# Kernel optimization log

Hardware: AMD Instinct MI355X
Metric: run time of the kernel (lower is better)

The kernel has to match this reference:

```python
import jax, jax.numpy as jnp
import numpy as np

EMBED = 1024
HEADS = 16
HEAD_DIM = EMBED // HEADS
MAX_REL = 16


def setup_inputs() -> dict:
    key = jax.random.key(0)
    ks = jax.random.split(key, 8)
    s = 0.02
    x = jax.random.normal(ks[0], (4, 2048, EMBED), dtype=jnp.float32)
    Wq = jax.random.normal(ks[1], (EMBED, EMBED), dtype=jnp.float32) * s
    bq = jnp.zeros((EMBED,), dtype=jnp.float32)
    Wk = jax.random.normal(ks[2], (EMBED, EMBED), dtype=jnp.float32) * s
    bk = jnp.zeros((EMBED,), dtype=jnp.float32)
    Wv = jax.random.normal(ks[3], (EMBED, EMBED), dtype=jnp.float32) * s
    bv = jnp.zeros((EMBED,), dtype=jnp.float32)
    rel_bias = jax.random.normal(ks[4], (2 * MAX_REL + 1, HEADS), dtype=jnp.float32) * s
    return {"x": x, "Wq": Wq, "bq": bq, "Wk": Wk, "bk": bk, "Wv": Wv, "bv": bv, "rel_bias": rel_bias}


def reference(x, Wq, bq, Wk, bk, Wv, bv, rel_bias):
    B, S, _ = x.shape
    # projections (Linear: x @ W + b, with W stored [in, out])
    q = (x @ Wq + bq).reshape(B, S, HEADS, HEAD_DIM).transpose(0, 2, 1, 3)  # [B,H,S,D]
    k = (x @ Wk + bk).reshape(B, S, HEADS, HEAD_DIM).transpose(0, 2, 1, 3)
    v = (x @ Wv + bv).reshape(B, S, HEADS, HEAD_DIM).transpose(0, 2, 1, 3)
    scores = jnp.einsum('bhqd,bhkd->bhqk', q, k) / jnp.sqrt(jnp.float32(HEAD_DIM))
    pos = jnp.arange(S)
    rel = jnp.clip(pos[None, :] - pos[:, None], -MAX_REL, MAX_REL) + MAX_REL  # [S,S]
    bias = rel_bias[rel]                      # [S,S,H]
    scores = scores + bias.transpose(2, 0, 1)[None]  # [B,H,S,S]
    probs = jax.nn.softmax(scores, axis=-1)
    # dropout is identity in eval mode
    out = jnp.einsum('bhqk,bhkd->bhqd', probs, v)
    return out.transpose(0, 2, 1, 3).reshape(B, S, EMBED)
```

## Files before the change

### kernel.cpp

```cpp
#include <hip/hip_runtime.h>

#define EMBED 1024
#define HEADS 16
#define HDIM  64
#define SEQ   2048
#define BATCH 4
#define MTOT  (BATCH*SEQ)

typedef __attribute__((ext_vector_type(8)))  short short8;
typedef __attribute__((ext_vector_type(4)))  float f32x4;
typedef __attribute__((ext_vector_type(16))) float f32x16;

#define GLOAD_LDS16(g, l) \
  __builtin_amdgcn_global_load_lds((const __attribute__((address_space(1))) void*)(g), \
                                   (__attribute__((address_space(3))) void*)(l), 16, 0, 0)

__device__ inline unsigned short f2bf(float f) {
  union { float f; unsigned u; } v; v.f = f;
  unsigned r = v.u + 0x7FFF + ((v.u >> 16) & 1);
  return (unsigned short)(r >> 16);
}

__device__ inline unsigned cvtpk(float lo, float hi) {
  unsigned r;
  asm("v_cvt_pk_bf16_f32 %0, %1, %2" : "=v"(r) : "v"(lo), "v"(hi));
  return r;
}

__device__ inline float vexp2(float x) {
  float r;
  asm("v_exp_f32 %0, %1" : "=v"(r) : "v"(x));
  return r;
}

#define PLSWAP(a, b) asm("v_permlane32_swap_b32 %0, %1" : "+v"(a), "+v"(b))

__device__ inline short8 mk8(unsigned w0, unsigned w1, unsigned w2, unsigned w3) {
  union { unsigned u[4]; short8 s; } x;
  x.u[0] = w0; x.u[1] = w1; x.u[2] = w2; x.u[3] = w3;
  return x.s;
}

__global__ void cvt_x(const float* __restrict__ x, unsigned short* __restrict__ xb) {
  int i = (blockIdx.x * blockDim.x + threadIdx.x) * 8;
  f32x4 a = *(const f32x4*)(x + i);
  f32x4 b = *(const f32x4*)(x + i + 4);
  unsigned short o[8];
  o[0]=f2bf(a[0]); o[1]=f2bf(a[1]); o[2]=f2bf(a[2]); o[3]=f2bf(a[3]);
  o[4]=f2bf(b[0]); o[5]=f2bf(b[1]); o[6]=f2bf(b[2]); o[7]=f2bf(b[3]);
  *(short8*)(xb + i) = *(short8*)o;
}

__global__ void transpose_w(const float* __restrict__ Wq, const float* __restrict__ Wk,
                            const float* __restrict__ Wv, unsigned short* __restrict__ Wtb) {
  __shared__ float tile[32][33];
  int wsel = blockIdx.z;
  const float* W = wsel == 0 ? Wq : (wsel == 1 ? Wk : Wv);
  int k0 = blockIdx.x * 32, n0 = blockIdx.y * 32;
  int tx = threadIdx.x & 31, ty = threadIdx.x >> 5;
  for (int i = 0; i < 4; ++i)
    tile[ty + i*8][tx] = W[(k0 + ty + i*8) * EMBED + n0 + tx];
  __syncthreads();
  unsigned short* o = Wtb + wsel * EMBED * EMBED;
  for (int i = 0; i < 4; ++i)
    o[(n0 + ty + i*8) * EMBED + k0 + tx] = f2bf(tile[tx][ty + i*8]);
}

__global__ __launch_bounds__(256)
void qkv_gemm(const unsigned short* __restrict__ xb, const unsigned short* __restrict__ Wtb,
              const float* __restrict__ bq, const float* __restrict__ bk, const float* __restrict__ bv,
              unsigned short* __restrict__ Qb, unsigned short* __restrict__ Kb,
              unsigned short* __restrict__ Vt) {
  __shared__ unsigned short As[128 * 72];
  __shared__ unsigned short Bs[128 * 72];
  int wsel = blockIdx.z;
  int m0 = blockIdx.x * 128, n0 = blockIdx.y * 128;
  int t = threadIdx.x, lane = t & 63, wave = t >> 6;
  int wr = wave >> 1, wc = wave & 1;
  int lr = lane & 15, lg = lane >> 4;
  const unsigned short* Wt = Wtb + wsel * (EMBED * EMBED);
  const float* bias = wsel == 0 ? bq : (wsel == 1 ? bk : bv);

  f32x4 acc[4][4] = {};

  for (int kt = 0; kt < EMBED / 64; ++kt) {
    int k0 = kt * 64;
    for (int i = 0; i < 4; ++i) {
      int c = i * 256 + t;
      int row = c >> 3, col8 = c & 7;
      short8 va = *(const short8*)(xb + (m0 + row) * EMBED + k0 + col8 * 8);
      short8 vb = *(const short8*)(Wt + (n0 + row) * EMBED + k0 + col8 * 8);
      *(short8*)(As + row * 72 + col8 * 8) = va;
      *(short8*)(Bs + row * 72 + col8 * 8) = vb;
    }
    __syncthreads();
    for (int kk = 0; kk < 2; ++kk) {
      short8 af[4], bfr[4];
      for (int mf = 0; mf < 4; ++mf)
        af[mf] = *(const short8*)(As + (wr * 64 + mf * 16 + lr) * 72 + kk * 32 + lg * 8);
      for (int nf = 0; nf < 4; ++nf)
        bfr[nf] = *(const short8*)(Bs + (wc * 64 + nf * 16 + lr) * 72 + kk * 32 + lg * 8);
      for (int mf = 0; mf < 4; ++mf)
        for (int nf = 0; nf < 4; ++nf)
          acc[mf][nf] = __builtin_amdgcn_mfma_f32_16x16x32_bf16(af[mf], bfr[nf], acc[mf][nf], 0, 0, 0);
    }
    __syncthreads();
  }

  const float SCLQ = 0.125f * 1.44269504088896340736f;
  for (int nf = 0; nf < 4; ++nf) {
    int n = n0 + wc * 64 + nf * 16 + lr;
    float bval = bias[n];
    int h = n >> 6, d = n & 63;
    for (int mf = 0; mf < 4; ++mf) {
      for (int r = 0; r < 4; ++r) {
        int m = m0 + wr * 64 + mf * 16 + lg * 4 + r;
        int b = m >> 11, s = m & 2047;
        float oval = acc[mf][nf][r] + bval;
        if (wsel == 0) oval *= SCLQ;
        unsigned short bfv = f2bf(oval);
        if (wsel == 0)      Qb[((b * HEADS + h) * SEQ + s) * HDIM + d] = bfv;
        else if (wsel == 1) Kb[((b * HEADS + h) * SEQ + s) * HDIM + d] = bfv;
        else                Vt[((b * HEADS + h) * HDIM + d) * SEQ + s] = bfv;
      }
    }
  }
}

__global__ __launch_bounds__(256)
void attn(const unsigned short* __restrict__ Qb, const unsigned short* __restrict__ Kb,
          const unsigned short* __restrict__ Vt, const float* __restrict__ rel_bias,
          float* __restrict__ out) {
  __shared__ unsigned short KVs[24576];
  __shared__ float bias_l[33];
  __shared__ float dld[4][32];
  int lid = ((blockIdx.x & 7) << 7) + (blockIdx.x >> 3);
  int bh = lid >> 4;
  int qb = lid & 15;
  int b = bh >> 4, h = bh & 15;
  int t = threadIdx.x, lane = t & 63, wave = t >> 6;
  int l31 = lane & 31, hi = lane >> 5;
  const float LOG2E = 1.44269504088896340736f;
  if (t < 33) bias_l[t] = rel_bias[t * HEADS + h] * LOG2E;

  int qw0 = qb * 128 + wave * 32;
  const unsigned short* Qp = Qb + (bh * SEQ + qw0) * HDIM;
  const unsigned short* Kp = Kb + bh * SEQ * HDIM;
  const unsigned short* Vp = Vt + bh * HDIM * SEQ;

  short8 qf[4];
  #pragma unroll
  for (int ks = 0; ks < 4; ++ks)
    qf[ks] = *(const short8*)(Qp + l31 * HDIM + ks * 16 + hi * 8);

  unsigned rbo[2][4];
  #pragma unroll
  for (int rs = 0; rs < 2; ++rs)
    #pragma unroll
    for (int ks = 0; ks < 4; ++ks) {
      int row = rs * 32 + l31;
      rbo[rs][ks] = (unsigned)((row << 7) + ((((ks << 1) | hi) ^ (row & 7)) << 4));
    }
  #define LDK(rs, ks, BUF) \
    (*(const short8*)((const char*)KVs + rbo[rs][ks] + (BUF) * 8192))
  #define LDVv(rs, ks, BUF) \
    (*(const short8*)((const char*)KVs + rbo[rs][ks] + 24576 + (BUF) * 8192))

  f32x16 O0 = {}, O1 = {};
  float ls0 = 0.f, ls1 = 0.f;
  int q = qw0 + l31;

  int srow0 = (wave << 4) + (lane >> 3);
  int sslot = lane & 7;

  #define STAGE(BUF, key0_)                                                          \
    for (int j = 0; j < 2; ++j) {                                                    \
      int srow = srow0 + j * 8;                                                      \
      int cs = sslot ^ (srow & 7);                                                   \
      GLOAD_LDS16(Kp + ((key0_) + srow) * HDIM + cs * 8,                             \
                  (char*)KVs + (BUF) * 8192 + ((((wave << 4) + j * 8) << 6) << 1));  \
      GLOAD_LDS16(Vp + srow * SEQ + (key0_) + cs * 8,                                \
                  (char*)KVs + 24576 + (BUF) * 8192 + ((((wave << 4) + j * 8) << 6) << 1)); \
    }

  #define WAITV4 asm volatile("s_waitcnt vmcnt(4)" ::: "memory");
  #define WAITV0 asm volatile("s_waitcnt vmcnt(0)" ::: "memory");
  #define BAR    __builtin_amdgcn_s_barrier();

  float cbLo, cbHi;

  #define PROC(SACC, KOFF, BUF)  {                                                   \
    float pv[16];                                                                    \
    int kbase = key0 + (KOFF);                                                       \
    if (kbase >= qw0 + 47) {                                                         \
      _Pragma("unroll") for (int r = 0; r < 16; ++r)                                 \
        pv[r] = vexp2(SACC[r] + cbHi);                                               \
    } else if (kbase <= qw0 - 47) {                                                  \
      _Pragma("unroll") for (int r = 0; r < 16; ++r)                                 \
        pv[r] = vexp2(SACC[r] + cbLo);                                               \
    } else {                                                                         \
      _Pragma("unroll") for (int r = 0; r < 16; ++r) {                               \
        int key = kbase + (r & 3) + 8 * (r >> 2) + 4 * hi;                           \
        int rel = key - q;                                                           \
        rel = rel < -16 ? -16 : (rel > 16 ? 16 : rel);                               \
        pv[r] = vexp2(SACC[r] + bias_l[rel + 16]);                                   \
      }                                                                              \
    }                                                                                \
    ls0 += ((pv[0] + pv[1]) + (pv[2] + pv[3])) + ((pv[4] + pv[5]) + (pv[6] + pv[7]));\
    ls1 += ((pv[8] + pv[9]) + (pv[10] + pv[11])) + ((pv[12] + pv[13]) + (pv[14] + pv[15]));\
    unsigned a0 = cvtpk(pv[0], pv[1]),  a1 = cvtpk(pv[4], pv[5]);   PLSWAP(a0, a1);  \
    unsigned a2 = cvtpk(pv[2], pv[3]),  a3 = cvtpk(pv[6], pv[7]);   PLSWAP(a2, a3);  \
    unsigned b0 = cvtpk(pv[8], pv[9]),  b1 = cvtpk(pv[12], pv[13]); PLSWAP(b0, b1);  \
    unsigned b2 = cvtpk(pv[10], pv[11]), b3 = cvtpk(pv[14], pv[15]); PLSWAP(b2, b3); \
    short8 pa0 = mk8(a0, a2, a1, a3);                                                \
    short8 pa1 = mk8(b0, b2, b1, b3);                                                \
    __builtin_amdgcn_s_setprio(1);                                                   \
    O0 = __builtin_amdgcn_mfma_f32_32x32x16_bf16(pa0, LDVv(0, (KOFF)/16, BUF),     O0, 0, 0, 0); \
    O1 = __builtin_amdgcn_mfma_f32_32x32x16_bf16(pa0, LDVv(1, (KOFF)/16, BUF),     O1, 0, 0, 0); \
    O0 = __builtin_amdgcn_mfma_f32_32x32x16_bf16(pa1, LDVv(0, (KOFF)/16 + 1, BUF), O0, 0, 0, 0); \
    O1 = __builtin_amdgcn_mfma_f32_32x32x16_bf16(pa1, LDVv(1, (KOFF)/16 + 1, BUF), O1, 0, 0, 0); \
    __builtin_amdgcn_s_setprio(0);                                                   \
  }

  #define HALF(RS, KOFF, BUF)  {                                                     \
    f32x16 s_ = {};                                                                  \
    __builtin_amdgcn_s_setprio(1);                                                   \
    _Pragma("unroll") for (int ks = 0; ks < 4; ++ks)                                 \
      s_ = __builtin_amdgcn_mfma_f32_32x32x16_bf16(LDK(RS, ks, BUF), qf[ks], s_, 0, 0, 0); \
    __builtin_amdgcn_s_setprio(0);                                                   \
    PROC(s_, KOFF, BUF)                                                              \
  }

  #define COMPUTE(BUF, KEY0)  {                                                      \
    int key0 = (KEY0);                                                               \
    HALF(0, 0, BUF)                                                                  \
    HALF(1, 32, BUF)                                                                 \
  }

  STAGE(0, 0)
  STAGE(1, 64)
  WAITV4
  __syncthreads();
  cbLo = bias_l[0]; cbHi = bias_l[32];

  for (int i = 0; i < 10; ++i) {
    int t3 = i * 3;
    STAGE(2, (t3 + 2) * 64)  COMPUTE(0, t3 * 64)        WAITV4 BAR
    STAGE(0, (t3 + 3) * 64)  COMPUTE(1, (t3 + 1) * 64)  WAITV4 BAR
    STAGE(1, (t3 + 4) * 64)  COMPUTE(2, (t3 + 2) * 64)  WAITV4 BAR
  }
  COMPUTE(0, 30 * 64)
  WAITV0 BAR
  COMPUTE(1, 31 * 64)

  float lsum = ls0 + ls1;
  float denom = lsum + __shfl_xor(lsum, 32, 64);
  if (lane < 32) dld[wave][l31] = 1.0f / denom;
  float* op = out + (b * SEQ + qw0) * EMBED + h * HDIM;
  #pragma unroll
  for (int r = 0; r < 16; ++r) {
    int ql = (r & 3) + 8 * (r >> 2) + 4 * hi;
    float inv = dld[wave][ql];
    op[ql * EMBED + l31]      = O0[r] * inv;
    op[ql * EMBED + 32 + l31] = O1[r] * inv;
  }
  #undef STAGE
  #undef LDK
  #undef LDVv
  #undef PROC
  #undef HALF
  #undef COMPUTE
}

extern "C" void kernel_launch(void* const* d_in, const int* in_sizes, int n_in,
                              void* d_out, int out_size, void* d_ws, size_t ws_size,
                              hipStream_t stream) {
  const float* x        = (const float*)d_in[0];
  const float* Wq       = (const float*)d_in[1];
  const float* bq       = (const float*)d_in[2];
  const float* Wk       = (const float*)d_in[3];
  const float* bk       = (const float*)d_in[4];
  const float* Wv       = (const float*)d_in[5];
  const float* bv       = (const float*)d_in[6];
  const float* rel_bias = (const float*)d_in[7];
  float* out = (float*)d_out;

  char* ws = (char*)d_ws;
  unsigned short* xb  = (unsigned short*)(ws);
  unsigned short* Wtb = (unsigned short*)(ws + 16777216);
  unsigned short* Qb  = (unsigned short*)(ws + 23068672);
  unsigned short* Kb  = (unsigned short*)(ws + 39845888);
  unsigned short* Vt  = (unsigned short*)(ws + 56623104);

  cvt_x<<<MTOT * EMBED / (256 * 8), 256, 0, stream>>>(x, xb);
  transpose_w<<<dim3(32, 32, 3), 256, 0, stream>>>(Wq, Wk, Wv, Wtb);
  qkv_gemm<<<dim3(MTOT / 128, EMBED / 128, 3), 256, 0, stream>>>(xb, Wtb, bq, bk, bv, Qb, Kb, Vt);
  attn<<<dim3(SEQ / 128 * BATCH * HEADS), 256, 0, stream>>>(Qb, Kb, Vt, rel_bias, out);
}
```

Measured before the change: 199.0 us.

## Fuse x conversion into QKV GEMM and restage attention with 128-key double buffer

Removes the separate cvt_x kernel and converts fp32 x to bf16 inside the QKV GEMM tile load. This saves one launch and the bf16 round trip, but each x tile is now read as fp32 and converted again by every N-block and weight selector (24 times). The attention kernel changes from a triple-buffered 64-key pipeline to a double-buffered 128-key pipeline with a new swizzled V layout and full __syncthreads barriers instead of vmcnt waits. This gives fewer barriers per key but larger LDS use and less latency hiding.

```diff
diff --git a/kernel.cpp b/kernel.cpp
--- a/kernel.cpp
+++ b/kernel.cpp
@@ -39,16 +39,6 @@
   union { unsigned u[4]; short8 s; } x;
   x.u[0] = w0; x.u[1] = w1; x.u[2] = w2; x.u[3] = w3;
   return x.s;
-}
-
-__global__ void cvt_x(const float* __restrict__ x, unsigned short* __restrict__ xb) {
-  int i = (blockIdx.x * blockDim.x + threadIdx.x) * 8;
-  f32x4 a = *(const f32x4*)(x + i);
-  f32x4 b = *(const f32x4*)(x + i + 4);
-  unsigned short o[8];
-  o[0]=f2bf(a[0]); o[1]=f2bf(a[1]); o[2]=f2bf(a[2]); o[3]=f2bf(a[3]);
-  o[4]=f2bf(b[0]); o[5]=f2bf(b[1]); o[6]=f2bf(b[2]); o[7]=f2bf(b[3]);
-  *(short8*)(xb + i) = *(short8*)o;
 }
 
 __global__ void transpose_w(const float* __restrict__ Wq, const float* __restrict__ Wk,
@@ -67,7 +57,7 @@
 }
 
 __global__ __launch_bounds__(256)
-void qkv_gemm(const unsigned short* __restrict__ xb, const unsigned short* __restrict__ Wtb,
+void qkv_gemm(const float* __restrict__ x, const unsigned short* __restrict__ Wtb,
               const float* __restrict__ bq, const float* __restrict__ bk, const float* __restrict__ bv,
               unsigned short* __restrict__ Qb, unsigned short* __restrict__ Kb,
               unsigned short* __restrict__ Vt) {
@@ -88,9 +78,14 @@
     for (int i = 0; i < 4; ++i) {
       int c = i * 256 + t;
       int row = c >> 3, col8 = c & 7;
-      short8 va = *(const short8*)(xb + (m0 + row) * EMBED + k0 + col8 * 8);
+      const float* xr = x + (m0 + row) * EMBED + k0 + col8 * 8;
+      f32x4 a0 = *(const f32x4*)xr;
+      f32x4 a1 = *(const f32x4*)(xr + 4);
+      unsigned short o[8];
+      o[0]=f2bf(a0[0]); o[1]=f2bf(a0[1]); o[2]=f2bf(a0[2]); o[3]=f2bf(a0[3]);
+      o[4]=f2bf(a1[0]); o[5]=f2bf(a1[1]); o[6]=f2bf(a1[2]); o[7]=f2bf(a1[3]);
       short8 vb = *(const short8*)(Wt + (n0 + row) * EMBED + k0 + col8 * 8);
-      *(short8*)(As + row * 72 + col8 * 8) = va;
+      *(short8*)(As + row * 72 + col8 * 8) = *(short8*)o;
       *(short8*)(Bs + row * 72 + col8 * 8) = vb;
     }
     __syncthreads();
@@ -131,7 +126,7 @@
 void attn(const unsigned short* __restrict__ Qb, const unsigned short* __restrict__ Kb,
           const unsigned short* __restrict__ Vt, const float* __restrict__ rel_bias,
           float* __restrict__ out) {
-  __shared__ unsigned short KVs[24576];
+  __shared__ unsigned short KVs[32768];
   __shared__ float bias_l[33];
   __shared__ float dld[4][32];
   int lid = ((blockIdx.x & 7) << 7) + (blockIdx.x >> 3);
@@ -153,41 +148,42 @@
   for (int ks = 0; ks < 4; ++ks)
     qf[ks] = *(const short8*)(Qp + l31 * HDIM + ks * 16 + hi * 8);
 
-  unsigned rbo[2][4];
+  unsigned rbo[4];
   #pragma unroll
-  for (int rs = 0; rs < 2; ++rs)
-    #pragma unroll
-    for (int ks = 0; ks < 4; ++ks) {
-      int row = rs * 32 + l31;
-      rbo[rs][ks] = (unsigned)((row << 7) + ((((ks << 1) | hi) ^ (row & 7)) << 4));
-    }
+  for (int ks = 0; ks < 4; ++ks)
+    rbo[ks] = (unsigned)((l31 << 7) + ((((ks << 1) | hi) ^ (l31 & 7)) << 4));
+  unsigned cHi = (unsigned)((l31 >> 1) & 3);
+  unsigned vb0 = (unsigned)(l31 * 256 + ((hi ^ (l31 & 1)) << 4));
+  unsigned vb1 = vb0 + 32 * 256;
+
   #define LDK(rs, ks, BUF) \
-    (*(const short8*)((const char*)KVs + rbo[rs][ks] + (BUF) * 8192))
-  #define LDVv(rs, ks, BUF) \
-    (*(const short8*)((const char*)KVs + rbo[rs][ks] + 24576 + (BUF) * 8192))
+    (*(const short8*)((const char*)KVs + rbo[ks] + (rs) * 4096 + (BUF) * 16384))
+  #define LDVv(rs, tt, BUF) \
+    (*(const short8*)((const char*)KVs + ((rs) == 0 ? vb0 : vb1) + \
+                      ((((tt) >> 1) ^ cHi) << 5) + 32768 + (BUF) * 16384))
 
   f32x16 O0 = {}, O1 = {};
   float ls0 = 0.f, ls1 = 0.f;
   int q = qw0 + l31;
 
-  int srow0 = (wave << 4) + (lane >> 3);
-  int sslot = lane & 7;
-
-  #define STAGE(BUF, key0_)                                                          \
-    for (int j = 0; j < 2; ++j) {                                                    \
-      int srow = srow0 + j * 8;                                                      \
-      int cs = sslot ^ (srow & 7);                                                   \
+  #define STAGE(BUF, key0_)  {                                                       \
+    for (int j = 0; j < 4; ++j) {                                                    \
+      int srow = (wave << 5) + j * 8 + (lane >> 3);                                  \
+      int cs = (lane & 7) ^ (srow & 7);                                              \
       GLOAD_LDS16(Kp + ((key0_) + srow) * HDIM + cs * 8,                             \
-                  (char*)KVs + (BUF) * 8192 + ((((wave << 4) + j * 8) << 6) << 1));  \
-      GLOAD_LDS16(Vp + srow * SEQ + (key0_) + cs * 8,                                \
-                  (char*)KVs + 24576 + (BUF) * 8192 + ((((wave << 4) + j * 8) << 6) << 1)); \
-    }
-
-  #define WAITV4 asm volatile("s_waitcnt vmcnt(4)" ::: "memory");
-  #define WAITV0 asm volatile("s_waitcnt vmcnt(0)" ::: "memory");
-  #define BAR    __builtin_amdgcn_s_barrier();
-
-  float cbLo, cbHi;
+                  (char*)KVs + (BUF) * 16384 + (((wave << 5) + j * 8) << 7));        \
+    }                                                                                \
+    for (int j = 0; j < 4; ++j) {                                                    \
+      int drow = (wave << 4) + j * 4 + (lane >> 4);                                  \
+      int cv = (lane & 15) ^ (drow & 7);                                             \
+      GLOAD_LDS16(Vp + drow * SEQ + (key0_) + cv * 8,                                \
+                  (char*)KVs + 32768 + (BUF) * 16384 + (((wave << 4) + j * 4) << 8));\
+    }                                                                                \
+  }
+
+  STAGE(0, 0)
+  __syncthreads();
+  float cbLo = bias_l[0], cbHi = bias_l[32];
 
   #define PROC(SACC, KOFF, BUF)  {                                                   \
     float pv[16];                                                                    \
@@ -215,43 +211,42 @@
     short8 pa0 = mk8(a0, a2, a1, a3);                                                \
     short8 pa1 = mk8(b0, b2, b1, b3);                                                \
     __builtin_amdgcn_s_setprio(1);                                                   \
-    O0 = __builtin_amdgcn_mfma_f32_32x32x16_bf16(pa0, LDVv(0, (KOFF)/16, BUF),     O0, 0, 0, 0); \
-    O1 = __builtin_amdgcn_mfma_f32_32x32x16_bf16(pa0, LDVv(1, (KOFF)/16, BUF),     O1, 0, 0, 0); \
-    O0 = __builtin_amdgcn_mfma_f32_32x32x16_bf16(pa1, LDVv(0, (KOFF)/16 + 1, BUF), O0, 0, 0, 0); \
-    O1 = __builtin_amdgcn_mfma_f32_32x32x16_bf16(pa1, LDVv(1, (KOFF)/16 + 1, BUF), O1, 0, 0, 0); \
+    O0 = __builtin_amdgcn_mfma_f32_32x32x16_bf16(pa0, LDVv(0, (KOFF) >> 3, BUF),       O0, 0, 0, 0); \
+    O1 = __builtin_amdgcn_mfma_f32_32x32x16_bf16(pa0, LDVv(1, (KOFF) >> 3, BUF),       O1, 0, 0, 0); \
+    O0 = __builtin_amdgcn_mfma_f32_32x32x16_bf16(pa1, LDVv(0, ((KOFF) >> 3) + 2, BUF), O0, 0, 0, 0); \
+    O1 = __builtin_amdgcn_mfma_f32_32x32x16_bf16(pa1, LDVv(1, ((KOFF) >> 3) + 2, BUF), O1, 0, 0, 0); \
     __builtin_amdgcn_s_setprio(0);                                                   \
   }
 
-  #define HALF(RS, KOFF, BUF)  {                                                     \
+  #define HALF(RS, BUF)  {                                                           \
     f32x16 s_ = {};                                                                  \
     __builtin_amdgcn_s_setprio(1);                                                   \
     _Pragma("unroll") for (int ks = 0; ks < 4; ++ks)                                 \
       s_ = __builtin_amdgcn_mfma_f32_32x32x16_bf16(LDK(RS, ks, BUF), qf[ks], s_, 0, 0, 0); \
     __builtin_amdgcn_s_setprio(0);                                                   \
-    PROC(s_, KOFF, BUF)                                                              \
+    PROC(s_, (RS) * 32, BUF)                                                         \
   }
 
   #define COMPUTE(BUF, KEY0)  {                                                      \
     int key0 = (KEY0);                                                               \
-    HALF(0, 0, BUF)                                                                  \
-    HALF(1, 32, BUF)                                                                 \
-  }
-
-  STAGE(0, 0)
-  STAGE(1, 64)
-  WAITV4
-  __syncthreads();
-  cbLo = bias_l[0]; cbHi = bias_l[32];
-
-  for (int i = 0; i < 10; ++i) {
-    int t3 = i * 3;
-    STAGE(2, (t3 + 2) * 64)  COMPUTE(0, t3 * 64)        WAITV4 BAR
-    STAGE(0, (t3 + 3) * 64)  COMPUTE(1, (t3 + 1) * 64)  WAITV4 BAR
-    STAGE(1, (t3 + 4) * 64)  COMPUTE(2, (t3 + 2) * 64)  WAITV4 BAR
-  }
-  COMPUTE(0, 30 * 64)
-  WAITV0 BAR
-  COMPUTE(1, 31 * 64)
+    HALF(0, BUF)                                                                     \
+    HALF(1, BUF)                                                                     \
+    HALF(2, BUF)                                                                     \
+    HALF(3, BUF)                                                                     \
+  }
+
+  for (int i = 0; i < 8; ++i) {
+    {
+      STAGE(1, (2 * i + 1) * 128)
+      COMPUTE(0, (2 * i) * 128)
+      __syncthreads();
+    }
+    {
+      if (i < 7) { STAGE(0, (2 * i + 2) * 128) }
+      COMPUTE(1, (2 * i + 1) * 128)
+      __syncthreads();
+    }
+  }
 
   float lsum = ls0 + ls1;
   float denom = lsum + __shfl_xor(lsum, 32, 64);
@@ -286,14 +281,12 @@
   float* out = (float*)d_out;
 
   char* ws = (char*)d_ws;
-  unsigned short* xb  = (unsigned short*)(ws);
   unsigned short* Wtb = (unsigned short*)(ws + 16777216);
   unsigned short* Qb  = (unsigned short*)(ws + 23068672);
   unsigned short* Kb  = (unsigned short*)(ws + 39845888);
   unsigned short* Vt  = (unsigned short*)(ws + 56623104);
 
-  cvt_x<<<MTOT * EMBED / (256 * 8), 256, 0, stream>>>(x, xb);
   transpose_w<<<dim3(32, 32, 3), 256, 0, stream>>>(Wq, Wk, Wv, Wtb);
-  qkv_gemm<<<dim3(MTOT / 128, EMBED / 128, 3), 256, 0, stream>>>(xb, Wtb, bq, bk, bv, Qb, Kb, Vt);
+  qkv_gemm<<<dim3(MTOT / 128, EMBED / 128, 3), 256, 0, stream>>>(x, Wtb, bq, bk, bv, Qb, Kb, Vt);
   attn<<<dim3(SEQ / 128 * BATCH * HEADS), 256, 0, stream>>>(Qb, Kb, Vt, rel_bias, out);
 }
```

New measurement: 252.7 us. 27.0% more time.

## Fuse x fp32-to-bf16 conversion into QKV GEMM and split softmax PV into halves

Applied to the files above, without the earlier changes.

Removes the standalone cvt_x kernel and converts x from fp32 to bf16 while loading tiles inside qkv_gemm. This saves a kernel launch and a 16 MB write plus re-read. In exchange, the GEMM now reads fp32 x, twice the bytes, for each of the 24 N/wsel tile columns that reuse it. The attention kernel also restructures its P·V processing into 8-element chunks with a single row-sum accumulator, and recomputes swizzled LDS addresses instead of keeping precomputed offset arrays. The aim there is lower register pressure and the ability to interleave exp work with MFMAs.

```diff
diff --git a/kernel.cpp b/kernel.cpp
--- a/kernel.cpp
+++ b/kernel.cpp
@@ -39,16 +39,6 @@
   union { unsigned u[4]; short8 s; } x;
   x.u[0] = w0; x.u[1] = w1; x.u[2] = w2; x.u[3] = w3;
   return x.s;
-}
-
-__global__ void cvt_x(const float* __restrict__ x, unsigned short* __restrict__ xb) {
-  int i = (blockIdx.x * blockDim.x + threadIdx.x) * 8;
-  f32x4 a = *(const f32x4*)(x + i);
-  f32x4 b = *(const f32x4*)(x + i + 4);
-  unsigned short o[8];
-  o[0]=f2bf(a[0]); o[1]=f2bf(a[1]); o[2]=f2bf(a[2]); o[3]=f2bf(a[3]);
-  o[4]=f2bf(b[0]); o[5]=f2bf(b[1]); o[6]=f2bf(b[2]); o[7]=f2bf(b[3]);
-  *(short8*)(xb + i) = *(short8*)o;
 }
 
 __global__ void transpose_w(const float* __restrict__ Wq, const float* __restrict__ Wk,
@@ -67,7 +57,7 @@
 }
 
 __global__ __launch_bounds__(256)
-void qkv_gemm(const unsigned short* __restrict__ xb, const unsigned short* __restrict__ Wtb,
+void qkv_gemm(const float* __restrict__ x, const unsigned short* __restrict__ Wtb,
               const float* __restrict__ bq, const float* __restrict__ bk, const float* __restrict__ bv,
               unsigned short* __restrict__ Qb, unsigned short* __restrict__ Kb,
               unsigned short* __restrict__ Vt) {
@@ -88,9 +78,14 @@
     for (int i = 0; i < 4; ++i) {
       int c = i * 256 + t;
       int row = c >> 3, col8 = c & 7;
-      short8 va = *(const short8*)(xb + (m0 + row) * EMBED + k0 + col8 * 8);
+      const float* xr = x + (m0 + row) * EMBED + k0 + col8 * 8;
+      f32x4 a0 = *(const f32x4*)xr;
+      f32x4 a1 = *(const f32x4*)(xr + 4);
+      unsigned short o[8];
+      o[0]=f2bf(a0[0]); o[1]=f2bf(a0[1]); o[2]=f2bf(a0[2]); o[3]=f2bf(a0[3]);
+      o[4]=f2bf(a1[0]); o[5]=f2bf(a1[1]); o[6]=f2bf(a1[2]); o[7]=f2bf(a1[3]);
       short8 vb = *(const short8*)(Wt + (n0 + row) * EMBED + k0 + col8 * 8);
-      *(short8*)(As + row * 72 + col8 * 8) = va;
+      *(short8*)(As + row * 72 + col8 * 8) = *(short8*)o;
       *(short8*)(Bs + row * 72 + col8 * 8) = vb;
     }
     __syncthreads();
@@ -153,21 +148,15 @@
   for (int ks = 0; ks < 4; ++ks)
     qf[ks] = *(const short8*)(Qp + l31 * HDIM + ks * 16 + hi * 8);
 
-  unsigned rbo[2][4];
-  #pragma unroll
-  for (int rs = 0; rs < 2; ++rs)
-    #pragma unroll
-    for (int ks = 0; ks < 4; ++ks) {
-      int row = rs * 32 + l31;
-      rbo[rs][ks] = (unsigned)((row << 7) + ((((ks << 1) | hi) ^ (row & 7)) << 4));
-    }
+  unsigned xa1 = (unsigned)((l31 & 7) >> 1);
+  unsigned lbase = (unsigned)((l31 << 7) + ((hi ^ (l31 & 1)) << 4));
   #define LDK(rs, ks, BUF) \
-    (*(const short8*)((const char*)KVs + rbo[rs][ks] + (BUF) * 8192))
-  #define LDVv(rs, ks, BUF) \
-    (*(const short8*)((const char*)KVs + rbo[rs][ks] + 24576 + (BUF) * 8192))
+    (*(const short8*)((const char*)KVs + lbase + (((ks) ^ xa1) << 5) + (rs) * 4096 + (BUF) * 8192))
+  #define LDV(rs, ks, BUF) \
+    (*(const short8*)((const char*)KVs + lbase + (((ks) ^ xa1) << 5) + (rs) * 4096 + 24576 + (BUF) * 8192))
 
   f32x16 O0 = {}, O1 = {};
-  float ls0 = 0.f, ls1 = 0.f;
+  float ls0 = 0.f;
   int q = qw0 + l31;
 
   int srow0 = (wave << 4) + (lane >> 3);
@@ -189,52 +178,48 @@
 
   float cbLo, cbHi;
 
-  #define PROC(SACC, KOFF, BUF)  {                                                   \
-    float pv[16];                                                                    \
-    int kbase = key0 + (KOFF);                                                       \
+  #define PROC8(SACC, RO, VKS, BUF)  {                                               \
+    float pv[8];                                                                     \
     if (kbase >= qw0 + 47) {                                                         \
-      _Pragma("unroll") for (int r = 0; r < 16; ++r)                                 \
-        pv[r] = vexp2(SACC[r] + cbHi);                                               \
+      _Pragma("unroll") for (int r = 0; r < 8; ++r)                                  \
+        pv[r] = vexp2(SACC[(RO) + r] + cbHi);                                        \
     } else if (kbase <= qw0 - 47) {                                                  \
-      _Pragma("unroll") for (int r = 0; r < 16; ++r)                                 \
-        pv[r] = vexp2(SACC[r] + cbLo);                                               \
+      _Pragma("unroll") for (int r = 0; r < 8; ++r)                                  \
+        pv[r] = vexp2(SACC[(RO) + r] + cbLo);                                        \
     } else {                                                                         \
-      _Pragma("unroll") for (int r = 0; r < 16; ++r) {                               \
-        int key = kbase + (r & 3) + 8 * (r >> 2) + 4 * hi;                           \
+      _Pragma("unroll") for (int r = 0; r < 8; ++r) {                                \
+        int rr = (RO) + r;                                                           \
+        int key = kbase + (rr & 3) + 8 * (rr >> 2) + 4 * hi;                         \
         int rel = key - q;                                                           \
         rel = rel < -16 ? -16 : (rel > 16 ? 16 : rel);                               \
-        pv[r] = vexp2(SACC[r] + bias_l[rel + 16]);                                   \
+        pv[r] = vexp2(SACC[rr] + bias_l[rel + 16]);                                  \
       }                                                                              \
     }                                                                                \
     ls0 += ((pv[0] + pv[1]) + (pv[2] + pv[3])) + ((pv[4] + pv[5]) + (pv[6] + pv[7]));\
-    ls1 += ((pv[8] + pv[9]) + (pv[10] + pv[11])) + ((pv[12] + pv[13]) + (pv[14] + pv[15]));\
     unsigned a0 = cvtpk(pv[0], pv[1]),  a1 = cvtpk(pv[4], pv[5]);   PLSWAP(a0, a1);  \
     unsigned a2 = cvtpk(pv[2], pv[3]),  a3 = cvtpk(pv[6], pv[7]);   PLSWAP(a2, a3);  \
-    unsigned b0 = cvtpk(pv[8], pv[9]),  b1 = cvtpk(pv[12], pv[13]); PLSWAP(b0, b1);  \
-    unsigned b2 = cvtpk(pv[10], pv[11]), b3 = cvtpk(pv[14], pv[15]); PLSWAP(b2, b3); \
-    short8 pa0 = mk8(a0, a2, a1, a3);                                                \
-    short8 pa1 = mk8(b0, b2, b1, b3);                                                \
+    short8 pa = mk8(a0, a2, a1, a3);                                                 \
     __builtin_amdgcn_s_setprio(1);                                                   \
-    O0 = __builtin_amdgcn_mfma_f32_32x32x16_bf16(pa0, LDVv(0, (KOFF)/16, BUF),     O0, 0, 0, 0); \
-    O1 = __builtin_amdgcn_mfma_f32_32x32x16_bf16(pa0, LDVv(1, (KOFF)/16, BUF),     O1, 0, 0, 0); \
-    O0 = __builtin_amdgcn_mfma_f32_32x32x16_bf16(pa1, LDVv(0, (KOFF)/16 + 1, BUF), O0, 0, 0, 0); \
-    O1 = __builtin_amdgcn_mfma_f32_32x32x16_bf16(pa1, LDVv(1, (KOFF)/16 + 1, BUF), O1, 0, 0, 0); \
+    O0 = __builtin_amdgcn_mfma_f32_32x32x16_bf16(pa, LDV(0, VKS, BUF), O0, 0, 0, 0); \
+    O1 = __builtin_amdgcn_mfma_f32_32x32x16_bf16(pa, LDV(1, VKS, BUF), O1, 0, 0, 0); \
     __builtin_amdgcn_s_setprio(0);                                                   \
   }
 
-  #define HALF(RS, KOFF, BUF)  {                                                     \
+  #define HALF(RS, BUF)  {                                                           \
     f32x16 s_ = {};                                                                  \
     __builtin_amdgcn_s_setprio(1);                                                   \
     _Pragma("unroll") for (int ks = 0; ks < 4; ++ks)                                 \
       s_ = __builtin_amdgcn_mfma_f32_32x32x16_bf16(LDK(RS, ks, BUF), qf[ks], s_, 0, 0, 0); \
     __builtin_amdgcn_s_setprio(0);                                                   \
-    PROC(s_, KOFF, BUF)                                                              \
+    int kbase = key0 + (RS) * 32;                                                    \
+    PROC8(s_, 0, (RS) * 2, BUF)                                                      \
+    PROC8(s_, 8, (RS) * 2 + 1, BUF)                                                  \
   }
 
   #define COMPUTE(BUF, KEY0)  {                                                      \
     int key0 = (KEY0);                                                               \
-    HALF(0, 0, BUF)                                                                  \
-    HALF(1, 32, BUF)                                                                 \
+    HALF(0, BUF)                                                                     \
+    HALF(1, BUF)                                                                     \
   }
 
   STAGE(0, 0)
@@ -253,8 +238,7 @@
   WAITV0 BAR
   COMPUTE(1, 31 * 64)
 
-  float lsum = ls0 + ls1;
-  float denom = lsum + __shfl_xor(lsum, 32, 64);
+  float denom = ls0 + __shfl_xor(ls0, 32, 64);
   if (lane < 32) dld[wave][l31] = 1.0f / denom;
   float* op = out + (b * SEQ + qw0) * EMBED + h * HDIM;
   #pragma unroll
@@ -266,8 +250,8 @@
   }
   #undef STAGE
   #undef LDK
-  #undef LDVv
-  #undef PROC
+  #undef LDV
+  #undef PROC8
   #undef HALF
   #undef COMPUTE
 }
@@ -286,14 +270,12 @@
   float* out = (float*)d_out;
 
   char* ws = (char*)d_ws;
-  unsigned short* xb  = (unsigned short*)(ws);
   unsigned short* Wtb = (unsigned short*)(ws + 16777216);
   unsigned short* Qb  = (unsigned short*)(ws + 23068672);
   unsigned short* Kb  = (unsigned short*)(ws + 39845888);
   unsigned short* Vt  = (unsigned short*)(ws + 56623104);
 
-  cvt_x<<<MTOT * EMBED / (256 * 8), 256, 0, stream>>>(x, xb);
   transpose_w<<<dim3(32, 32, 3), 256, 0, stream>>>(Wq, Wk, Wv, Wtb);
-  qkv_gemm<<<dim3(MTOT / 128, EMBED / 128, 3), 256, 0, stream>>>(xb, Wtb, bq, bk, bv, Qb, Kb, Vt);
+  qkv_gemm<<<dim3(MTOT / 128, EMBED / 128, 3), 256, 0, stream>>>(x, Wtb, bq, bk, bv, Qb, Kb, Vt);
   attn<<<dim3(SEQ / 128 * BATCH * HEADS), 256, 0, stream>>>(Qb, Kb, Vt, rel_bias, out);
 }
```

After: 209.7 us. +5.4%, slower.
